# Kernel tuning notes

Measured on AMD Instinct MI355X. Metric: run time of the kernel, lower is better.

The kernel has to match this reference:

```python
import jax, jax.numpy as jnp
import numpy as np

M_NODES = 49152  # HEALPix nside=64


def setup_inputs() -> dict:
    key = jax.random.key(0)
    ks = jax.random.split(key, 7)
    N, M, Fin, Fout, K, dm = 16, M_NODES, 32, 64, 5, 1
    E = 8 * M
    x = jax.random.normal(ks[0], (N, M, Fin), dtype=jnp.float32)
    # sparse Laplacian in COO form; small values keep Chebyshev recursion stable
    edge_vals = jax.random.normal(ks[1], (E,), dtype=jnp.float32) * 0.2
    edge_rows = jax.random.randint(ks[2], (E,), 0, M, dtype=jnp.int32)
    edge_cols = jax.random.randint(ks[3], (E,), 0, M, dtype=jnp.int32)
    dkernel = jax.random.normal(ks[4], (Fin, dm, K), dtype=jnp.float32) * (2.0 / K) ** 0.5
    pkernel = jax.random.normal(ks[5], (Fout, Fin * dm), dtype=jnp.float32) * (2.0 / (Fin * dm)) ** 0.5
    bias = jax.random.normal(ks[6], (1, 1, Fout), dtype=jnp.float32) * 0.01
    return {"x": x, "edge_vals": edge_vals, "dkernel": dkernel,
            "pkernel": pkernel, "bias": bias,
            "edge_rows": edge_rows, "edge_cols": edge_cols}


def reference(x, edge_vals, dkernel, pkernel, bias, edge_rows, edge_cols):
    N, M, Fin = x.shape
    _, dm, K = dkernel.shape
    Fout = pkernel.shape[0]

    def spmm(v):  # L @ v with L in COO, v: [M, C]
        return jax.ops.segment_sum(edge_vals[:, None] * v[edge_cols], edge_rows,
                                   num_segments=M)

    # x0: [M, N*Fin]
    x0 = jnp.transpose(x, (1, 0, 2)).reshape(M, N * Fin)
    stack = [x0]
    if K > 1:
        x1 = spmm(x0)
        stack.append(x1)
    for k in range(2, K):  # Chebyshev recursion T_k = 2 L T_{k-1} - T_{k-2}
        x2 = 2.0 * spmm(x1) - x0
        stack.append(x2)
        x0, x1 = x1, x2
    xs = jnp.stack(stack, axis=0)                      # [K, M, N*Fin]
    xs = xs.reshape(K, M, N, Fin)
    xs = jnp.transpose(xs, (3, 0, 2, 1)).reshape(Fin, K, N * M)
    y = jnp.einsum('fdk,fkp->fdp', dkernel, xs)        # depthwise: [Fin, dm, N*M]
    y = y.reshape(Fin * dm, N * M)
    y = pkernel @ y                                    # pointwise: [Fout, N*M]
    y = y.T.reshape(N, M, Fout)
    y = y + bias
    return jax.nn.relu(y)
```

## Files before the change

### kernel.cpp

```cpp
#include <hip/hip_runtime.h>


#define M_NODES 49152
#define FIN 32
#define KCH 5
#define FOUT 64
#define NB 16

typedef unsigned int u32;
typedef unsigned short u16;
typedef short bf16x8 __attribute__((ext_vector_type(8)));
typedef float f32x4 __attribute__((ext_vector_type(4)));

__device__ __forceinline__ float bflo(u32 w) { union { float f; u32 i; } v; v.i = w << 16; return v.f; }
__device__ __forceinline__ float bfhi(u32 w) { union { float f; u32 i; } v; v.i = w & 0xffff0000u; return v.f; }
__device__ __forceinline__ u32 f2bf(float f) {
    union { float f; u32 i; } v; v.f = f;
    u32 r = v.i + 0x7fffu + ((v.i >> 16) & 1u);
    return r >> 16;
}
__device__ __forceinline__ u32 pack2(float a, float b) { return f2bf(a) | (f2bf(b) << 16); }

__device__ __forceinline__ void stage_row(const uint4* gsrc, uint4* ldst) {
    __builtin_amdgcn_global_load_lds(
        (const __attribute__((address_space(1))) unsigned int*)gsrc,
        (__attribute__((address_space(3))) unsigned int*)ldst, 16, 0, 0);
}

__global__ void scatter_kernel(const int* __restrict__ rows, const int* __restrict__ cols,
                               const float* __restrict__ vals, int* __restrict__ cnt,
                               int2* __restrict__ ell, int E4) {
    int e = blockIdx.x * 256 + threadIdx.x;
    if (e < E4) {
        int4 r = ((const int4*)rows)[e];
        int4 c = ((const int4*)cols)[e];
        float4 v = ((const float4*)vals)[e];
        int pos;
        pos = atomicAdd(&cnt[r.x], 1); if (pos < 32) ell[(size_t)r.x * 32 + pos] = (int2){c.x, __float_as_int(v.x)};
        pos = atomicAdd(&cnt[r.y], 1); if (pos < 32) ell[(size_t)r.y * 32 + pos] = (int2){c.y, __float_as_int(v.y)};
        pos = atomicAdd(&cnt[r.z], 1); if (pos < 32) ell[(size_t)r.z * 32 + pos] = (int2){c.z, __float_as_int(v.z)};
        pos = atomicAdd(&cnt[r.w], 1); if (pos < 32) ell[(size_t)r.w * 32 + pos] = (int2){c.w, __float_as_int(v.w)};
    }
}

__global__ __launch_bounds__(256) void cast_transpose_kernel(
    const float* __restrict__ x, uint4* __restrict__ T0, int M) {
    int m = blockIdx.x * 4 + (threadIdx.x >> 6);
    int l = threadIdx.x & 63;
    int n = l >> 2;
    int f0 = (l & 3) * 8;
    const f32x4* xp = (const f32x4*)(x + ((size_t)n * M + m) * FIN + f0);
    f32x4 a = __builtin_nontemporal_load(xp);
    f32x4 b = __builtin_nontemporal_load(xp + 1);
    uint4 o;
    o.x = pack2(a[0], a[1]); o.y = pack2(a[2], a[3]);
    o.z = pack2(b[0], b[1]); o.w = pack2(b[2], b[3]);
    T0[(size_t)m * 64 + l] = o;
}

__global__ void wprep_kernel(const float* __restrict__ dk, const float* __restrict__ pk,
                             u16* __restrict__ W) {
    int t = blockIdx.x * 256 + threadIdx.x;
    if (t < FOUT * KCH * FIN) {
        int fo = t / (KCH * FIN);
        int kf = t % (KCH * FIN);
        int kc = kf / FIN;
        int f  = kf % FIN;
        W[fo * (KCH * FIN) + kf] = (u16)f2bf(pk[fo * FIN + f] * dk[f * KCH + kc]);
    }
}

__device__ __forceinline__ void acc8(float* r, uint4 g, float v) {
    r[0] = fmaf(v, bflo(g.x), r[0]); r[1] = fmaf(v, bfhi(g.x), r[1]);
    r[2] = fmaf(v, bflo(g.y), r[2]); r[3] = fmaf(v, bfhi(g.y), r[3]);
    r[4] = fmaf(v, bflo(g.z), r[4]); r[5] = fmaf(v, bfhi(g.z), r[5]);
    r[6] = fmaf(v, bflo(g.w), r[6]); r[7] = fmaf(v, bfhi(g.w), r[7]);
}

template<int FIRST>
__global__ __launch_bounds__(256) void spmm_kernel(
    const uint4* __restrict__ Tin, const uint4* __restrict__ Tprev, uint4* __restrict__ Tout,
    const int* __restrict__ deg, const int2* __restrict__ ell, int M) {
    int w = __builtin_amdgcn_readfirstlane((int)(threadIdx.x >> 6));
    int l = threadIdx.x & 63;
    int rA = blockIdx.x * 8 + w * 2;
    int rB = rA + 1;
    int dA = deg[rA]; if (dA > 32) dA = 32;
    int dB = deg[rB]; if (dB > 32) dB = 32;
    const int2* eA = ell + (size_t)rA * 32;
    const int2* eB = ell + (size_t)rB * 32;
    uint4 pA, pB;
    if (!FIRST) {
        pA = Tprev[(size_t)rA * 64 + l];
        pB = Tprev[(size_t)rB * 64 + l];
    }
    float a[8] = {0.f, 0.f, 0.f, 0.f, 0.f, 0.f, 0.f, 0.f};
    float b[8] = {0.f, 0.f, 0.f, 0.f, 0.f, 0.f, 0.f, 0.f};
    int dmax = dA > dB ? dA : dB;
    for (int s = 0; s < dmax; s += 8) {
        int cA = dA - s, cB = dB - s;
        int2 edA[8], edB[8];
        uint4 gA[8], gB[8];
        #pragma unroll
        for (int j = 0; j < 8; ++j) if (j < cA) edA[j] = eA[s + j];
        #pragma unroll
        for (int j = 0; j < 8; ++j) if (j < cB) edB[j] = eB[s + j];
        #pragma unroll
        for (int j = 0; j < 8; ++j) if (j < cA) gA[j] = Tin[(size_t)edA[j].x * 64 + l];
        #pragma unroll
        for (int j = 0; j < 8; ++j) if (j < cB) gB[j] = Tin[(size_t)edB[j].x * 64 + l];
        #pragma unroll
        for (int j = 0; j < 8; ++j) if (j < cA) acc8(a, gA[j], __int_as_float(edA[j].y));
        #pragma unroll
        for (int j = 0; j < 8; ++j) if (j < cB) acc8(b, gB[j], __int_as_float(edB[j].y));
    }
    if (!FIRST) {
        a[0] = fmaf(2.f, a[0], -bflo(pA.x)); a[1] = fmaf(2.f, a[1], -bfhi(pA.x));
        a[2] = fmaf(2.f, a[2], -bflo(pA.y)); a[3] = fmaf(2.f, a[3], -bfhi(pA.y));
        a[4] = fmaf(2.f, a[4], -bflo(pA.z)); a[5] = fmaf(2.f, a[5], -bfhi(pA.z));
        a[6] = fmaf(2.f, a[6], -bflo(pA.w)); a[7] = fmaf(2.f, a[7], -bfhi(pA.w));
        b[0] = fmaf(2.f, b[0], -bflo(pB.x)); b[1] = fmaf(2.f, b[1], -bfhi(pB.x));
        b[2] = fmaf(2.f, b[2], -bflo(pB.y)); b[3] = fmaf(2.f, b[3], -bfhi(pB.y));
        b[4] = fmaf(2.f, b[4], -bflo(pB.z)); b[5] = fmaf(2.f, b[5], -bfhi(pB.z));
        b[6] = fmaf(2.f, b[6], -bflo(pB.w)); b[7] = fmaf(2.f, b[7], -bfhi(pB.w));
    }
    uint4 oA, oB;
    oA.x = pack2(a[0], a[1]); oA.y = pack2(a[2], a[3]);
    oA.z = pack2(a[4], a[5]); oA.w = pack2(a[6], a[7]);
    oB.x = pack2(b[0], b[1]); oB.y = pack2(b[2], b[3]);
    oB.z = pack2(b[4], b[5]); oB.w = pack2(b[6], b[7]);
    Tout[(size_t)rA * 64 + l] = oA;
    Tout[(size_t)rB * 64 + l] = oB;
}

__global__ __launch_bounds__(256) void pw_mfma_kernel(
    const uint4* __restrict__ T, const uint4* __restrict__ W4,
    const float* __restrict__ bias, float* __restrict__ out, int M) {
    __shared__ uint4 lds4[5 * 1024];
    int t = threadIdx.x;
    int w = t >> 6;
    int l = t & 63;
    int lr = l & 15;
    int lg = l >> 4;
    int m0 = blockIdx.x * 16;
    const size_t kstride = (size_t)M * 64;

    bf16x8 bfr[KCH][4];
    #pragma unroll
    for (int kc = 0; kc < KCH; ++kc)
        #pragma unroll
        for (int fo = 0; fo < 4; ++fo) {
            uint4 wv = W4[(fo * 16 + lr) * 20 + kc * 4 + lg];
            bfr[kc][fo] = *(bf16x8*)&wv;
        }
    f32x4 acc[4][4];
    #pragma unroll
    for (int fo = 0; fo < 4; ++fo) {
        float bv = bias[fo * 16 + lr];
        #pragma unroll
        for (int nn = 0; nn < 4; ++nn)
            acc[nn][fo] = (f32x4){bv, bv, bv, bv};
    }

    #pragma unroll
    for (int kc = 0; kc < KCH; ++kc) {
        #pragma unroll
        for (int i = 0; i < 4; ++i) {
            int row = w * 4 + i;
            const uint4* gsrc = T + (size_t)kc * kstride + (size_t)(m0 + row) * 64
                                  + (l ^ (row & 7));
            stage_row(gsrc, &lds4[kc * 1024 + row * 64]);
        }
    }
    __syncthreads();

    #pragma unroll
    for (int kc = 0; kc < KCH; ++kc) {
        #pragma unroll
        for (int nn = 0; nn < 4; ++nn) {
            int n = w * 4 + nn;
            uint4 a = lds4[kc * 1024 + lr * 64 + ((n * 4 + lg) ^ (lr & 7))];
            bf16x8 af = *(bf16x8*)&a;
            #pragma unroll
            for (int fo = 0; fo < 4; ++fo)
                acc[nn][fo] = __builtin_amdgcn_mfma_f32_16x16x32_bf16(af, bfr[kc][fo], acc[nn][fo], 0, 0, 0);
        }
    }
    __syncthreads();

    float* zone = (float*)lds4 + w * 1088;
    #pragma unroll
    for (int nn = 0; nn < 4; ++nn) {
        int n = w * 4 + nn;
        #pragma unroll
        for (int fo = 0; fo < 4; ++fo)
            #pragma unroll
            for (int rr = 0; rr < 4; ++rr)
                zone[(lg * 4 + rr) * 68 + fo * 16 + lr] = acc[nn][fo][rr];
        #pragma unroll
        for (int i = 0; i < 4; ++i) {
            int mrow = i * 4 + lg;
            f32x4 v = *(const f32x4*)&zone[mrow * 68 + lr * 4];
            v[0] = fmaxf(v[0], 0.f); v[1] = fmaxf(v[1], 0.f);
            v[2] = fmaxf(v[2], 0.f); v[3] = fmaxf(v[3], 0.f);
            f32x4* op = (f32x4*)(out + ((size_t)n * M + m0 + mrow) * FOUT + lr * 4);
            __builtin_nontemporal_store(v, op);
        }
    }
}

extern "C" void kernel_launch(void* const* d_in, const int* in_sizes, int n_in,
                              void* d_out, int out_size, void* d_ws, size_t ws_size,
                              hipStream_t stream) {
    const float* x         = (const float*)d_in[0];
    const float* edge_vals = (const float*)d_in[1];
    const float* dk        = (const float*)d_in[2];
    const float* pk        = (const float*)d_in[3];
    const float* bias      = (const float*)d_in[4];
    const int*   erow      = (const int*)d_in[5];
    const int*   ecol      = (const int*)d_in[6];
    float* out = (float*)d_out;

    const int M = M_NODES;
    const int E = in_sizes[1];

    size_t t_words = (size_t)M * 64;
    uint4* T    = (uint4*)d_ws;
    u16*   W    = (u16*)(T + 5 * t_words);
    int*   deg  = (int*)(W + FOUT * KCH * FIN);
    int2*  ell  = (int2*)(deg + M);

    uint4* T0 = T;
    uint4* T1 = T + 1 * t_words;
    uint4* T2 = T + 2 * t_words;
    uint4* T3 = T + 3 * t_words;
    uint4* T4 = T + 4 * t_words;

    hipMemsetAsync(deg, 0, (size_t)M * sizeof(int), stream);
    scatter_kernel<<<(E / 4 + 255) / 256, 256, 0, stream>>>(erow, ecol, edge_vals, deg, ell, E / 4);

    cast_transpose_kernel<<<M / 4, 256, 0, stream>>>(x, T0, M);
    wprep_kernel<<<(FOUT * KCH * FIN + 255) / 256, 256, 0, stream>>>(dk, pk, W);

    spmm_kernel<1><<<M / 8, 256, 0, stream>>>(T0, T0, T1, deg, ell, M);
    spmm_kernel<0><<<M / 8, 256, 0, stream>>>(T1, T0, T2, deg, ell, M);
    spmm_kernel<0><<<M / 8, 256, 0, stream>>>(T2, T1, T3, deg, ell, M);
    spmm_kernel<0><<<M / 8, 256, 0, stream>>>(T3, T2, T4, deg, ell, M);

    pw_mfma_kernel<<<M / 16, 256, 0, stream>>>(T, (const uint4*)W, bias, out, M);
}
```

Before: 415.8 us.

## Reorder T into batch-group slices and split SpMM by group for cache locality

Changes the Chebyshev T buffers from node-major [M][N*Fin] to batch-slice-major [N][M][Fin] layout, so the input cast becomes a plain elementwise cast with no transpose. Each SpMM pass is split into two launches over halves of the batch, so the gathered working set per launch is smaller and more likely to stay in cache. SpMM now spreads a row's edges over four lane groups and reduces them with shuffles. ELL entries are packed into 32 bits as a 16-bit column plus a bf16 value, which truncates edge values to bf16 and limits column indices to 16 bits. The pointwise kernel's staging addresses are adjusted to read the new layout.

```diff
diff --git a/kernel.cpp b/kernel.cpp
--- a/kernel.cpp
+++ b/kernel.cpp
@@ -11,6 +11,7 @@
 typedef unsigned short u16;
 typedef short bf16x8 __attribute__((ext_vector_type(8)));
 typedef float f32x4 __attribute__((ext_vector_type(4)));
+typedef unsigned int u32x4 __attribute__((ext_vector_type(4)));
 
 __device__ __forceinline__ float bflo(u32 w) { union { float f; u32 i; } v; v.i = w << 16; return v.f; }
 __device__ __forceinline__ float bfhi(u32 w) { union { float f; u32 i; } v; v.i = w & 0xffff0000u; return v.f; }
@@ -20,6 +21,11 @@
     return r >> 16;
 }
 __device__ __forceinline__ u32 pack2(float a, float b) { return f2bf(a) | (f2bf(b) << 16); }
+__device__ __forceinline__ u32 cvtpk(float lo, float hi) {
+    u32 r;
+    asm("v_cvt_pk_bf16_f32 %0, %1, %2" : "=v"(r) : "v"(lo), "v"(hi));
+    return r;
+}
 
 __device__ __forceinline__ void stage_row(const uint4* gsrc, uint4* ldst) {
     __builtin_amdgcn_global_load_lds(
@@ -29,33 +35,32 @@
 
 __global__ void scatter_kernel(const int* __restrict__ rows, const int* __restrict__ cols,
                                const float* __restrict__ vals, int* __restrict__ cnt,
-                               int2* __restrict__ ell, int E4) {
+                               u32* __restrict__ ell, int E4) {
     int e = blockIdx.x * 256 + threadIdx.x;
     if (e < E4) {
         int4 r = ((const int4*)rows)[e];
         int4 c = ((const int4*)cols)[e];
         float4 v = ((const float4*)vals)[e];
         int pos;
-        pos = atomicAdd(&cnt[r.x], 1); if (pos < 32) ell[(size_t)r.x * 32 + pos] = (int2){c.x, __float_as_int(v.x)};
-        pos = atomicAdd(&cnt[r.y], 1); if (pos < 32) ell[(size_t)r.y * 32 + pos] = (int2){c.y, __float_as_int(v.y)};
-        pos = atomicAdd(&cnt[r.z], 1); if (pos < 32) ell[(size_t)r.z * 32 + pos] = (int2){c.z, __float_as_int(v.z)};
-        pos = atomicAdd(&cnt[r.w], 1); if (pos < 32) ell[(size_t)r.w * 32 + pos] = (int2){c.w, __float_as_int(v.w)};
-    }
-}
-
-__global__ __launch_bounds__(256) void cast_transpose_kernel(
-    const float* __restrict__ x, uint4* __restrict__ T0, int M) {
-    int m = blockIdx.x * 4 + (threadIdx.x >> 6);
-    int l = threadIdx.x & 63;
-    int n = l >> 2;
-    int f0 = (l & 3) * 8;
-    const f32x4* xp = (const f32x4*)(x + ((size_t)n * M + m) * FIN + f0);
-    f32x4 a = __builtin_nontemporal_load(xp);
-    f32x4 b = __builtin_nontemporal_load(xp + 1);
-    uint4 o;
-    o.x = pack2(a[0], a[1]); o.y = pack2(a[2], a[3]);
-    o.z = pack2(b[0], b[1]); o.w = pack2(b[2], b[3]);
-    T0[(size_t)m * 64 + l] = o;
+        pos = atomicAdd(&cnt[r.x], 1); if (pos < 32) ell[(size_t)r.x * 32 + pos] = (u32)(c.x & 0xFFFF) | (f2bf(v.x) << 16);
+        pos = atomicAdd(&cnt[r.y], 1); if (pos < 32) ell[(size_t)r.y * 32 + pos] = (u32)(c.y & 0xFFFF) | (f2bf(v.y) << 16);
+        pos = atomicAdd(&cnt[r.z], 1); if (pos < 32) ell[(size_t)r.z * 32 + pos] = (u32)(c.z & 0xFFFF) | (f2bf(v.z) << 16);
+        pos = atomicAdd(&cnt[r.w], 1); if (pos < 32) ell[(size_t)r.w * 32 + pos] = (u32)(c.w & 0xFFFF) | (f2bf(v.w) << 16);
+    }
+}
+
+__global__ __launch_bounds__(256) void cast_kernel(const float* __restrict__ x,
+                                                   uint4* __restrict__ T0, int n8) {
+    int i = blockIdx.x * 256 + threadIdx.x;
+    if (i < n8) {
+        const f32x4* xp = (const f32x4*)(x + (size_t)i * 8);
+        f32x4 a = __builtin_nontemporal_load(xp);
+        f32x4 b = __builtin_nontemporal_load(xp + 1);
+        uint4 o;
+        o.x = pack2(a[0], a[1]); o.y = pack2(a[2], a[3]);
+        o.z = pack2(b[0], b[1]); o.w = pack2(b[2], b[3]);
+        T0[i] = o;
+    }
 }
 
 __global__ void wprep_kernel(const float* __restrict__ dk, const float* __restrict__ pk,
@@ -70,67 +75,61 @@
     }
 }
 
-__device__ __forceinline__ void acc8(float* r, uint4 g, float v) {
-    r[0] = fmaf(v, bflo(g.x), r[0]); r[1] = fmaf(v, bfhi(g.x), r[1]);
-    r[2] = fmaf(v, bflo(g.y), r[2]); r[3] = fmaf(v, bfhi(g.y), r[3]);
-    r[4] = fmaf(v, bflo(g.z), r[4]); r[5] = fmaf(v, bfhi(g.z), r[5]);
-    r[6] = fmaf(v, bflo(g.w), r[6]); r[7] = fmaf(v, bfhi(g.w), r[7]);
-}
-
 template<int FIRST>
 __global__ __launch_bounds__(256) void spmm_kernel(
     const uint4* __restrict__ Tin, const uint4* __restrict__ Tprev, uint4* __restrict__ Tout,
-    const int* __restrict__ deg, const int2* __restrict__ ell, int M) {
-    int w = __builtin_amdgcn_readfirstlane((int)(threadIdx.x >> 6));
-    int l = threadIdx.x & 63;
-    int rA = blockIdx.x * 8 + w * 2;
-    int rB = rA + 1;
-    int dA = deg[rA]; if (dA > 32) dA = 32;
-    int dB = deg[rB]; if (dB > 32) dB = 32;
-    const int2* eA = ell + (size_t)rA * 32;
-    const int2* eB = ell + (size_t)rB * 32;
-    uint4 pA, pB;
-    if (!FIRST) {
-        pA = Tprev[(size_t)rA * 64 + l];
-        pB = Tprev[(size_t)rB * 64 + l];
-    }
-    float a[8] = {0.f, 0.f, 0.f, 0.f, 0.f, 0.f, 0.f, 0.f};
-    float b[8] = {0.f, 0.f, 0.f, 0.f, 0.f, 0.f, 0.f, 0.f};
-    int dmax = dA > dB ? dA : dB;
-    for (int s = 0; s < dmax; s += 8) {
-        int cA = dA - s, cB = dB - s;
-        int2 edA[8], edB[8];
-        uint4 gA[8], gB[8];
-        #pragma unroll
-        for (int j = 0; j < 8; ++j) if (j < cA) edA[j] = eA[s + j];
-        #pragma unroll
-        for (int j = 0; j < 8; ++j) if (j < cB) edB[j] = eB[s + j];
-        #pragma unroll
-        for (int j = 0; j < 8; ++j) if (j < cA) gA[j] = Tin[(size_t)edA[j].x * 64 + l];
-        #pragma unroll
-        for (int j = 0; j < 8; ++j) if (j < cB) gB[j] = Tin[(size_t)edB[j].x * 64 + l];
-        #pragma unroll
-        for (int j = 0; j < 8; ++j) if (j < cA) acc8(a, gA[j], __int_as_float(edA[j].y));
-        #pragma unroll
-        for (int j = 0; j < 8; ++j) if (j < cB) acc8(b, gB[j], __int_as_float(edB[j].y));
-    }
-    if (!FIRST) {
-        a[0] = fmaf(2.f, a[0], -bflo(pA.x)); a[1] = fmaf(2.f, a[1], -bfhi(pA.x));
-        a[2] = fmaf(2.f, a[2], -bflo(pA.y)); a[3] = fmaf(2.f, a[3], -bfhi(pA.y));
-        a[4] = fmaf(2.f, a[4], -bflo(pA.z)); a[5] = fmaf(2.f, a[5], -bfhi(pA.z));
-        a[6] = fmaf(2.f, a[6], -bflo(pA.w)); a[7] = fmaf(2.f, a[7], -bfhi(pA.w));
-        b[0] = fmaf(2.f, b[0], -bflo(pB.x)); b[1] = fmaf(2.f, b[1], -bfhi(pB.x));
-        b[2] = fmaf(2.f, b[2], -bflo(pB.y)); b[3] = fmaf(2.f, b[3], -bfhi(pB.y));
-        b[4] = fmaf(2.f, b[4], -bflo(pB.z)); b[5] = fmaf(2.f, b[5], -bfhi(pB.z));
-        b[6] = fmaf(2.f, b[6], -bflo(pB.w)); b[7] = fmaf(2.f, b[7], -bfhi(pB.w));
-    }
-    uint4 oA, oB;
-    oA.x = pack2(a[0], a[1]); oA.y = pack2(a[2], a[3]);
-    oA.z = pack2(a[4], a[5]); oA.w = pack2(a[6], a[7]);
-    oB.x = pack2(b[0], b[1]); oB.y = pack2(b[2], b[3]);
-    oB.z = pack2(b[4], b[5]); oB.w = pack2(b[6], b[7]);
-    Tout[(size_t)rA * 64 + l] = oA;
-    Tout[(size_t)rB * 64 + l] = oB;
+    const int* __restrict__ deg, const u32* __restrict__ ell, int gbase) {
+    const int M = M_NODES;
+    int t = threadIdx.x;
+    int l = t & 63;
+    int w = t >> 6;
+    int g = gbase + (blockIdx.x & 7);
+    int r = ((blockIdx.x >> 3) << 4) + (w << 2) + (l >> 4);
+    int j = (l >> 2) & 3;
+    int c = l & 3;
+    int d = deg[r]; if (d > 32) d = 32;
+    const u32* erow = ell + ((size_t)r << 5);
+    size_t sbase = (size_t)g * M * 4;
+    size_t srow  = sbase + (size_t)r * 4;
+
+    u32x4 p;
+    if (!FIRST) p = __builtin_nontemporal_load((const u32x4*)&Tprev[srow + c]);
+
+    float acc[8] = {0.f, 0.f, 0.f, 0.f, 0.f, 0.f, 0.f, 0.f};
+    for (int s = 0; s < d; s += 4) {
+        int mine = s + j;
+        u32 desc = 0;
+        if (mine < d) desc = __builtin_nontemporal_load(&erow[mine]);
+        float v = bfhi(desc);
+        int col = desc & 0xFFFF;
+        uint4 gv = {0, 0, 0, 0};
+        if (mine < d) gv = Tin[sbase + (size_t)col * 4 + c];
+        acc[0] = fmaf(v, bflo(gv.x), acc[0]); acc[1] = fmaf(v, bfhi(gv.x), acc[1]);
+        acc[2] = fmaf(v, bflo(gv.y), acc[2]); acc[3] = fmaf(v, bfhi(gv.y), acc[3]);
+        acc[4] = fmaf(v, bflo(gv.z), acc[4]); acc[5] = fmaf(v, bfhi(gv.z), acc[5]);
+        acc[6] = fmaf(v, bflo(gv.w), acc[6]); acc[7] = fmaf(v, bfhi(gv.w), acc[7]);
+    }
+    #pragma unroll
+    for (int q = 0; q < 8; ++q) acc[q] += __shfl_xor(acc[q], 4, 64);
+    #pragma unroll
+    for (int q = 0; q < 8; ++q) acc[q] += __shfl_xor(acc[q], 8, 64);
+
+    if (j == 0) {
+        float rr[8];
+        if (FIRST) {
+            #pragma unroll
+            for (int q = 0; q < 8; ++q) rr[q] = acc[q];
+        } else {
+            rr[0] = fmaf(2.f, acc[0], -bflo(p[0])); rr[1] = fmaf(2.f, acc[1], -bfhi(p[0]));
+            rr[2] = fmaf(2.f, acc[2], -bflo(p[1])); rr[3] = fmaf(2.f, acc[3], -bfhi(p[1]));
+            rr[4] = fmaf(2.f, acc[4], -bflo(p[2])); rr[5] = fmaf(2.f, acc[5], -bfhi(p[2]));
+            rr[6] = fmaf(2.f, acc[6], -bflo(p[3])); rr[7] = fmaf(2.f, acc[7], -bfhi(p[3]));
+        }
+        u32x4 o;
+        o[0] = cvtpk(rr[0], rr[1]); o[1] = cvtpk(rr[2], rr[3]);
+        o[2] = cvtpk(rr[4], rr[5]); o[3] = cvtpk(rr[6], rr[7]);
+        __builtin_nontemporal_store(o, (u32x4*)&Tout[srow + c]);
+    }
 }
 
 __global__ __launch_bounds__(256) void pw_mfma_kernel(
@@ -143,7 +142,8 @@
     int lr = l & 15;
     int lg = l >> 4;
     int m0 = blockIdx.x * 16;
-    const size_t kstride = (size_t)M * 64;
+    const size_t tslice = (size_t)M * 4;
+    const size_t kstride = tslice * 16;
 
     bf16x8 bfr[KCH][4];
     #pragma unroll
@@ -164,11 +164,12 @@
 
     #pragma unroll
     for (int kc = 0; kc < KCH; ++kc) {
+        const uint4* tk = T + (size_t)kc * kstride;
         #pragma unroll
         for (int i = 0; i < 4; ++i) {
             int row = w * 4 + i;
-            const uint4* gsrc = T + (size_t)kc * kstride + (size_t)(m0 + row) * 64
-                                  + (l ^ (row & 7));
+            int q = l ^ (row & 7);
+            const uint4* gsrc = tk + (size_t)(q >> 2) * tslice + (size_t)(m0 + row) * 4 + (q & 3);
             stage_row(gsrc, &lds4[kc * 1024 + row * 64]);
         }
     }
@@ -224,28 +225,34 @@
     const int M = M_NODES;
     const int E = in_sizes[1];
 
-    size_t t_words = (size_t)M * 64;
+    size_t t_u4 = (size_t)M * 4 * 16;
     uint4* T    = (uint4*)d_ws;
-    u16*   W    = (u16*)(T + 5 * t_words);
+    u16*   W    = (u16*)(T + 5 * t_u4);
     int*   deg  = (int*)(W + FOUT * KCH * FIN);
-    int2*  ell  = (int2*)(deg + M);
+    u32*   ell  = (u32*)(deg + M);
 
     uint4* T0 = T;
-    uint4* T1 = T + 1 * t_words;
-    uint4* T2 = T + 2 * t_words;
-    uint4* T3 = T + 3 * t_words;
-    uint4* T4 = T + 4 * t_words;
+    uint4* T1 = T + 1 * t_u4;
+    uint4* T2 = T + 2 * t_u4;
+    uint4* T3 = T + 3 * t_u4;
+    uint4* T4 = T + 4 * t_u4;
 
     hipMemsetAsync(deg, 0, (size_t)M * sizeof(int), stream);
     scatter_kernel<<<(E / 4 + 255) / 256, 256, 0, stream>>>(erow, ecol, edge_vals, deg, ell, E / 4);
 
-    cast_transpose_kernel<<<M / 4, 256, 0, stream>>>(x, T0, M);
+    int n8 = NB * M * FIN / 8;
+    cast_kernel<<<(n8 + 255) / 256, 256, 0, stream>>>(x, T0, n8);
     wprep_kernel<<<(FOUT * KCH * FIN + 255) / 256, 256, 0, stream>>>(dk, pk, W);
 
-    spmm_kernel<1><<<M / 8, 256, 0, stream>>>(T0, T0, T1, deg, ell, M);
-    spmm_kernel<0><<<M / 8, 256, 0, stream>>>(T1, T0, T2, deg, ell, M);
-    spmm_kernel<0><<<M / 8, 256, 0, stream>>>(T2, T1, T3, deg, ell, M);
-    spmm_kernel<0><<<M / 8, 256, 0, stream>>>(T3, T2, T4, deg, ell, M);
+    const int sgrid = 8 * (M / 16);
+    spmm_kernel<1><<<sgrid, 256, 0, stream>>>(T0, T0, T1, deg, ell, 0);
+    spmm_kernel<1><<<sgrid, 256, 0, stream>>>(T0, T0, T1, deg, ell, 8);
+    spmm_kernel<0><<<sgrid, 256, 0, stream>>>(T1, T0, T2, deg, ell, 0);
+    spmm_kernel<0><<<sgrid, 256, 0, stream>>>(T1, T0, T2, deg, ell, 8);
+    spmm_kernel<0><<<sgrid, 256, 0, stream>>>(T2, T1, T3, deg, ell, 0);
+    spmm_kernel<0><<<sgrid, 256, 0, stream>>>(T2, T1, T3, deg, ell, 8);
+    spmm_kernel<0><<<sgrid, 256, 0, stream>>>(T3, T2, T4, deg, ell, 0);
+    spmm_kernel<0><<<sgrid, 256, 0, stream>>>(T3, T2, T4, deg, ell, 8);
 
     pw_mfma_kernel<<<M / 16, 256, 0, stream>>>(T, (const uint4*)W, bias, out, M);
 }
```

New measurement: 690.5 us. 1.66x slower.

## Pack ELL entries into 32 bits and restructure pointwise MFMA per output slice

Applied to the files above, without the earlier changes.

ELL entries shrink from an int2 (column, fp32 value) to one u32 holding a 16-bit column index and a bf16 value, halving index traffic in the four SpMM passes. This relies on M fitting in 16 bits, which holds since 49152 < 65536, and it rounds the Laplacian values to bf16. The pointwise MFMA kernel drops the LDS staging of all K slices. Each wave now owns 16 output features and loops over the 16 batch entries, loading A fragments straight from global memory and using a small double-buffered LDS zone for the output transpose. This cuts LDS use and register pressure, at the cost of possibly less coalesced A loads.

```diff
diff --git a/kernel.cpp b/kernel.cpp
--- a/kernel.cpp
+++ b/kernel.cpp
@@ -21,25 +21,19 @@
 }
 __device__ __forceinline__ u32 pack2(float a, float b) { return f2bf(a) | (f2bf(b) << 16); }
 
-__device__ __forceinline__ void stage_row(const uint4* gsrc, uint4* ldst) {
-    __builtin_amdgcn_global_load_lds(
-        (const __attribute__((address_space(1))) unsigned int*)gsrc,
-        (__attribute__((address_space(3))) unsigned int*)ldst, 16, 0, 0);
-}
-
 __global__ void scatter_kernel(const int* __restrict__ rows, const int* __restrict__ cols,
                                const float* __restrict__ vals, int* __restrict__ cnt,
-                               int2* __restrict__ ell, int E4) {
+                               u32* __restrict__ ell, int E4) {
     int e = blockIdx.x * 256 + threadIdx.x;
     if (e < E4) {
         int4 r = ((const int4*)rows)[e];
         int4 c = ((const int4*)cols)[e];
         float4 v = ((const float4*)vals)[e];
         int pos;
-        pos = atomicAdd(&cnt[r.x], 1); if (pos < 32) ell[(size_t)r.x * 32 + pos] = (int2){c.x, __float_as_int(v.x)};
-        pos = atomicAdd(&cnt[r.y], 1); if (pos < 32) ell[(size_t)r.y * 32 + pos] = (int2){c.y, __float_as_int(v.y)};
-        pos = atomicAdd(&cnt[r.z], 1); if (pos < 32) ell[(size_t)r.z * 32 + pos] = (int2){c.z, __float_as_int(v.z)};
-        pos = atomicAdd(&cnt[r.w], 1); if (pos < 32) ell[(size_t)r.w * 32 + pos] = (int2){c.w, __float_as_int(v.w)};
+        pos = atomicAdd(&cnt[r.x], 1); if (pos < 32) ell[(size_t)r.x * 32 + pos] = (u32)(c.x & 0xFFFF) | (f2bf(v.x) << 16);
+        pos = atomicAdd(&cnt[r.y], 1); if (pos < 32) ell[(size_t)r.y * 32 + pos] = (u32)(c.y & 0xFFFF) | (f2bf(v.y) << 16);
+        pos = atomicAdd(&cnt[r.z], 1); if (pos < 32) ell[(size_t)r.z * 32 + pos] = (u32)(c.z & 0xFFFF) | (f2bf(v.z) << 16);
+        pos = atomicAdd(&cnt[r.w], 1); if (pos < 32) ell[(size_t)r.w * 32 + pos] = (u32)(c.w & 0xFFFF) | (f2bf(v.w) << 16);
     }
 }
 
@@ -80,15 +74,15 @@
 template<int FIRST>
 __global__ __launch_bounds__(256) void spmm_kernel(
     const uint4* __restrict__ Tin, const uint4* __restrict__ Tprev, uint4* __restrict__ Tout,
-    const int* __restrict__ deg, const int2* __restrict__ ell, int M) {
+    const int* __restrict__ deg, const u32* __restrict__ ell, int M) {
     int w = __builtin_amdgcn_readfirstlane((int)(threadIdx.x >> 6));
     int l = threadIdx.x & 63;
     int rA = blockIdx.x * 8 + w * 2;
     int rB = rA + 1;
     int dA = deg[rA]; if (dA > 32) dA = 32;
     int dB = deg[rB]; if (dB > 32) dB = 32;
-    const int2* eA = ell + (size_t)rA * 32;
-    const int2* eB = ell + (size_t)rB * 32;
+    const u32* eA = ell + ((size_t)rA << 5);
+    const u32* eB = ell + ((size_t)rB << 5);
     uint4 pA, pB;
     if (!FIRST) {
         pA = Tprev[(size_t)rA * 64 + l];
@@ -99,20 +93,20 @@
     int dmax = dA > dB ? dA : dB;
     for (int s = 0; s < dmax; s += 8) {
         int cA = dA - s, cB = dB - s;
-        int2 edA[8], edB[8];
+        u32 edA[8], edB[8];
         uint4 gA[8], gB[8];
         #pragma unroll
         for (int j = 0; j < 8; ++j) if (j < cA) edA[j] = eA[s + j];
         #pragma unroll
         for (int j = 0; j < 8; ++j) if (j < cB) edB[j] = eB[s + j];
         #pragma unroll
-        for (int j = 0; j < 8; ++j) if (j < cA) gA[j] = Tin[(size_t)edA[j].x * 64 + l];
-        #pragma unroll
-        for (int j = 0; j < 8; ++j) if (j < cB) gB[j] = Tin[(size_t)edB[j].x * 64 + l];
-        #pragma unroll
-        for (int j = 0; j < 8; ++j) if (j < cA) acc8(a, gA[j], __int_as_float(edA[j].y));
-        #pragma unroll
-        for (int j = 0; j < 8; ++j) if (j < cB) acc8(b, gB[j], __int_as_float(edB[j].y));
+        for (int j = 0; j < 8; ++j) if (j < cA) gA[j] = Tin[(size_t)(edA[j] & 0xFFFF) * 64 + l];
+        #pragma unroll
+        for (int j = 0; j < 8; ++j) if (j < cB) gB[j] = Tin[(size_t)(edB[j] & 0xFFFF) * 64 + l];
+        #pragma unroll
+        for (int j = 0; j < 8; ++j) if (j < cA) acc8(a, gA[j], bfhi(edA[j]));
+        #pragma unroll
+        for (int j = 0; j < 8; ++j) if (j < cB) acc8(b, gB[j], bfhi(edB[j]));
     }
     if (!FIRST) {
         a[0] = fmaf(2.f, a[0], -bflo(pA.x)); a[1] = fmaf(2.f, a[1], -bfhi(pA.x));
@@ -136,76 +130,47 @@
 __global__ __launch_bounds__(256) void pw_mfma_kernel(
     const uint4* __restrict__ T, const uint4* __restrict__ W4,
     const float* __restrict__ bias, float* __restrict__ out, int M) {
-    __shared__ uint4 lds4[5 * 1024];
+    __shared__ float zone[4 * 640];
     int t = threadIdx.x;
     int w = t >> 6;
     int l = t & 63;
     int lr = l & 15;
     int lg = l >> 4;
     int m0 = blockIdx.x * 16;
+    int fo0 = w * 16;
     const size_t kstride = (size_t)M * 64;
 
-    bf16x8 bfr[KCH][4];
-    #pragma unroll
-    for (int kc = 0; kc < KCH; ++kc)
-        #pragma unroll
-        for (int fo = 0; fo < 4; ++fo) {
-            uint4 wv = W4[(fo * 16 + lr) * 20 + kc * 4 + lg];
-            bfr[kc][fo] = *(bf16x8*)&wv;
-        }
-    f32x4 acc[4][4];
-    #pragma unroll
-    for (int fo = 0; fo < 4; ++fo) {
-        float bv = bias[fo * 16 + lr];
-        #pragma unroll
-        for (int nn = 0; nn < 4; ++nn)
-            acc[nn][fo] = (f32x4){bv, bv, bv, bv};
-    }
-
+    bf16x8 bfr[KCH];
     #pragma unroll
     for (int kc = 0; kc < KCH; ++kc) {
-        #pragma unroll
-        for (int i = 0; i < 4; ++i) {
-            int row = w * 4 + i;
-            const uint4* gsrc = T + (size_t)kc * kstride + (size_t)(m0 + row) * 64
-                                  + (l ^ (row & 7));
-            stage_row(gsrc, &lds4[kc * 1024 + row * 64]);
-        }
-    }
-    __syncthreads();
-
-    #pragma unroll
-    for (int kc = 0; kc < KCH; ++kc) {
-        #pragma unroll
-        for (int nn = 0; nn < 4; ++nn) {
-            int n = w * 4 + nn;
-            uint4 a = lds4[kc * 1024 + lr * 64 + ((n * 4 + lg) ^ (lr & 7))];
-            bf16x8 af = *(bf16x8*)&a;
-            #pragma unroll
-            for (int fo = 0; fo < 4; ++fo)
-                acc[nn][fo] = __builtin_amdgcn_mfma_f32_16x16x32_bf16(af, bfr[kc][fo], acc[nn][fo], 0, 0, 0);
-        }
-    }
-    __syncthreads();
-
-    float* zone = (float*)lds4 + w * 1088;
-    #pragma unroll
-    for (int nn = 0; nn < 4; ++nn) {
-        int n = w * 4 + nn;
-        #pragma unroll
-        for (int fo = 0; fo < 4; ++fo)
-            #pragma unroll
-            for (int rr = 0; rr < 4; ++rr)
-                zone[(lg * 4 + rr) * 68 + fo * 16 + lr] = acc[nn][fo][rr];
-        #pragma unroll
-        for (int i = 0; i < 4; ++i) {
-            int mrow = i * 4 + lg;
-            f32x4 v = *(const f32x4*)&zone[mrow * 68 + lr * 4];
-            v[0] = fmaxf(v[0], 0.f); v[1] = fmaxf(v[1], 0.f);
-            v[2] = fmaxf(v[2], 0.f); v[3] = fmaxf(v[3], 0.f);
-            f32x4* op = (f32x4*)(out + ((size_t)n * M + m0 + mrow) * FOUT + lr * 4);
-            __builtin_nontemporal_store(v, op);
-        }
+        uint4 wv = W4[(fo0 + lr) * 20 + kc * 4 + lg];
+        bfr[kc] = *(bf16x8*)&wv;
+    }
+    float bv = bias[fo0 + lr];
+    const uint4* abase = T + (size_t)(m0 + lr) * 64 + lg;
+    float* zbase = zone + w * 640;
+    int zr = l >> 2;
+    int zc = (l & 3) * 4;
+
+    #pragma unroll 2
+    for (int n = 0; n < NB; ++n) {
+        uint4 a[KCH];
+        #pragma unroll
+        for (int kc = 0; kc < KCH; ++kc)
+            a[kc] = abase[(size_t)kc * kstride + n * 4];
+        f32x4 acc = {bv, bv, bv, bv};
+        #pragma unroll
+        for (int kc = 0; kc < KCH; ++kc)
+            acc = __builtin_amdgcn_mfma_f32_16x16x32_bf16(*(bf16x8*)&a[kc], bfr[kc], acc, 0, 0, 0);
+        float* zw = zbase + (n & 1) * 320;
+        #pragma unroll
+        for (int rr = 0; rr < 4; ++rr)
+            zw[(lg * 4 + rr) * 20 + lr] = acc[rr];
+        f32x4 v = *(const f32x4*)&zw[zr * 20 + zc];
+        v[0] = fmaxf(v[0], 0.f); v[1] = fmaxf(v[1], 0.f);
+        v[2] = fmaxf(v[2], 0.f); v[3] = fmaxf(v[3], 0.f);
+        f32x4* op = (f32x4*)(out + ((size_t)n * M + m0 + zr) * FOUT + fo0 + zc);
+        __builtin_nontemporal_store(v, op);
     }
 }
 
@@ -228,7 +193,7 @@
     uint4* T    = (uint4*)d_ws;
     u16*   W    = (u16*)(T + 5 * t_words);
     int*   deg  = (int*)(W + FOUT * KCH * FIN);
-    int2*  ell  = (int2*)(deg + M);
+    u32*   ell  = (u32*)(deg + M);
 
     uint4* T0 = T;
     uint4* T1 = T + 1 * t_words;
```

New measurement: 461.2 us. 1.11x slower.

## Pack ELL entries into 32-bit index+bf16 value and widen pointwise blocks to 512

Applied to the files above, without the earlier changes.

Each ELL entry shrinks from an int2 to a single 32-bit word holding a 16-bit column index and a bf16 edge value. This halves the edge-list bytes the four SpMM passes read. The pointwise MFMA kernel now runs 512 threads per block, so each wave handles two batch rows instead of four, and weight fragments are loaded per Chebyshev order rather than held all at once, which lowers register pressure. The trade-offs are a coarser edge value in bf16 and column indices that only fit because M is at most 65536.

```diff
diff --git a/kernel.cpp b/kernel.cpp
--- a/kernel.cpp
+++ b/kernel.cpp
@@ -29,17 +29,17 @@
 
 __global__ void scatter_kernel(const int* __restrict__ rows, const int* __restrict__ cols,
                                const float* __restrict__ vals, int* __restrict__ cnt,
-                               int2* __restrict__ ell, int E4) {
+                               u32* __restrict__ ell, int E4) {
     int e = blockIdx.x * 256 + threadIdx.x;
     if (e < E4) {
         int4 r = ((const int4*)rows)[e];
         int4 c = ((const int4*)cols)[e];
         float4 v = ((const float4*)vals)[e];
         int pos;
-        pos = atomicAdd(&cnt[r.x], 1); if (pos < 32) ell[(size_t)r.x * 32 + pos] = (int2){c.x, __float_as_int(v.x)};
-        pos = atomicAdd(&cnt[r.y], 1); if (pos < 32) ell[(size_t)r.y * 32 + pos] = (int2){c.y, __float_as_int(v.y)};
-        pos = atomicAdd(&cnt[r.z], 1); if (pos < 32) ell[(size_t)r.z * 32 + pos] = (int2){c.z, __float_as_int(v.z)};
-        pos = atomicAdd(&cnt[r.w], 1); if (pos < 32) ell[(size_t)r.w * 32 + pos] = (int2){c.w, __float_as_int(v.w)};
+        pos = atomicAdd(&cnt[r.x], 1); if (pos < 32) ell[(size_t)r.x * 32 + pos] = (u32)(c.x & 0xFFFF) | (f2bf(v.x) << 16);
+        pos = atomicAdd(&cnt[r.y], 1); if (pos < 32) ell[(size_t)r.y * 32 + pos] = (u32)(c.y & 0xFFFF) | (f2bf(v.y) << 16);
+        pos = atomicAdd(&cnt[r.z], 1); if (pos < 32) ell[(size_t)r.z * 32 + pos] = (u32)(c.z & 0xFFFF) | (f2bf(v.z) << 16);
+        pos = atomicAdd(&cnt[r.w], 1); if (pos < 32) ell[(size_t)r.w * 32 + pos] = (u32)(c.w & 0xFFFF) | (f2bf(v.w) << 16);
     }
 }
 
@@ -80,15 +80,15 @@
 template<int FIRST>
 __global__ __launch_bounds__(256) void spmm_kernel(
     const uint4* __restrict__ Tin, const uint4* __restrict__ Tprev, uint4* __restrict__ Tout,
-    const int* __restrict__ deg, const int2* __restrict__ ell, int M) {
+    const int* __restrict__ deg, const u32* __restrict__ ell, int M) {
     int w = __builtin_amdgcn_readfirstlane((int)(threadIdx.x >> 6));
     int l = threadIdx.x & 63;
     int rA = blockIdx.x * 8 + w * 2;
     int rB = rA + 1;
     int dA = deg[rA]; if (dA > 32) dA = 32;
     int dB = deg[rB]; if (dB > 32) dB = 32;
-    const int2* eA = ell + (size_t)rA * 32;
-    const int2* eB = ell + (size_t)rB * 32;
+    const u32* eA = ell + ((size_t)rA << 5);
+    const u32* eB = ell + ((size_t)rB << 5);
     uint4 pA, pB;
     if (!FIRST) {
         pA = Tprev[(size_t)rA * 64 + l];
@@ -99,20 +99,20 @@
     int dmax = dA > dB ? dA : dB;
     for (int s = 0; s < dmax; s += 8) {
         int cA = dA - s, cB = dB - s;
-        int2 edA[8], edB[8];
+        u32 edA[8], edB[8];
         uint4 gA[8], gB[8];
         #pragma unroll
         for (int j = 0; j < 8; ++j) if (j < cA) edA[j] = eA[s + j];
         #pragma unroll
         for (int j = 0; j < 8; ++j) if (j < cB) edB[j] = eB[s + j];
         #pragma unroll
-        for (int j = 0; j < 8; ++j) if (j < cA) gA[j] = Tin[(size_t)edA[j].x * 64 + l];
-        #pragma unroll
-        for (int j = 0; j < 8; ++j) if (j < cB) gB[j] = Tin[(size_t)edB[j].x * 64 + l];
-        #pragma unroll
-        for (int j = 0; j < 8; ++j) if (j < cA) acc8(a, gA[j], __int_as_float(edA[j].y));
-        #pragma unroll
-        for (int j = 0; j < 8; ++j) if (j < cB) acc8(b, gB[j], __int_as_float(edB[j].y));
+        for (int j = 0; j < 8; ++j) if (j < cA) gA[j] = Tin[(size_t)(edA[j] & 0xFFFF) * 64 + l];
+        #pragma unroll
+        for (int j = 0; j < 8; ++j) if (j < cB) gB[j] = Tin[(size_t)(edB[j] & 0xFFFF) * 64 + l];
+        #pragma unroll
+        for (int j = 0; j < 8; ++j) if (j < cA) acc8(a, gA[j], bfhi(edA[j]));
+        #pragma unroll
+        for (int j = 0; j < 8; ++j) if (j < cB) acc8(b, gB[j], bfhi(edB[j]));
     }
     if (!FIRST) {
         a[0] = fmaf(2.f, a[0], -bflo(pA.x)); a[1] = fmaf(2.f, a[1], -bfhi(pA.x));
@@ -133,7 +133,7 @@
     Tout[(size_t)rB * 64 + l] = oB;
 }
 
-__global__ __launch_bounds__(256) void pw_mfma_kernel(
+__global__ __launch_bounds__(512, 4) void pw_mfma_kernel(
     const uint4* __restrict__ T, const uint4* __restrict__ W4,
     const float* __restrict__ bias, float* __restrict__ out, int M) {
     __shared__ uint4 lds4[5 * 1024];
@@ -145,53 +145,51 @@
     int m0 = blockIdx.x * 16;
     const size_t kstride = (size_t)M * 64;
 
-    bf16x8 bfr[KCH][4];
-    #pragma unroll
-    for (int kc = 0; kc < KCH; ++kc)
-        #pragma unroll
-        for (int fo = 0; fo < 4; ++fo) {
-            uint4 wv = W4[(fo * 16 + lr) * 20 + kc * 4 + lg];
-            bfr[kc][fo] = *(bf16x8*)&wv;
-        }
-    f32x4 acc[4][4];
-    #pragma unroll
-    for (int fo = 0; fo < 4; ++fo) {
-        float bv = bias[fo * 16 + lr];
-        #pragma unroll
-        for (int nn = 0; nn < 4; ++nn)
-            acc[nn][fo] = (f32x4){bv, bv, bv, bv};
-    }
-
     #pragma unroll
     for (int kc = 0; kc < KCH; ++kc) {
         #pragma unroll
-        for (int i = 0; i < 4; ++i) {
-            int row = w * 4 + i;
+        for (int i = 0; i < 2; ++i) {
+            int row = w * 2 + i;
             const uint4* gsrc = T + (size_t)kc * kstride + (size_t)(m0 + row) * 64
                                   + (l ^ (row & 7));
             stage_row(gsrc, &lds4[kc * 1024 + row * 64]);
         }
     }
+
+    f32x4 acc[2][4];
+    #pragma unroll
+    for (int fo = 0; fo < 4; ++fo) {
+        float bv = bias[fo * 16 + lr];
+        #pragma unroll
+        for (int nn = 0; nn < 2; ++nn)
+            acc[nn][fo] = (f32x4){bv, bv, bv, bv};
+    }
     __syncthreads();
 
     #pragma unroll
     for (int kc = 0; kc < KCH; ++kc) {
-        #pragma unroll
-        for (int nn = 0; nn < 4; ++nn) {
-            int n = w * 4 + nn;
+        bf16x8 bfr[4];
+        #pragma unroll
+        for (int fo = 0; fo < 4; ++fo) {
+            uint4 wv = W4[(fo * 16 + lr) * 20 + kc * 4 + lg];
+            bfr[fo] = *(bf16x8*)&wv;
+        }
+        #pragma unroll
+        for (int nn = 0; nn < 2; ++nn) {
+            int n = w * 2 + nn;
             uint4 a = lds4[kc * 1024 + lr * 64 + ((n * 4 + lg) ^ (lr & 7))];
             bf16x8 af = *(bf16x8*)&a;
             #pragma unroll
             for (int fo = 0; fo < 4; ++fo)
-                acc[nn][fo] = __builtin_amdgcn_mfma_f32_16x16x32_bf16(af, bfr[kc][fo], acc[nn][fo], 0, 0, 0);
+                acc[nn][fo] = __builtin_amdgcn_mfma_f32_16x16x32_bf16(af, bfr[fo], acc[nn][fo], 0, 0, 0);
         }
     }
     __syncthreads();
 
     float* zone = (float*)lds4 + w * 1088;
     #pragma unroll
-    for (int nn = 0; nn < 4; ++nn) {
-        int n = w * 4 + nn;
+    for (int nn = 0; nn < 2; ++nn) {
+        int n = w * 2 + nn;
         #pragma unroll
         for (int fo = 0; fo < 4; ++fo)
             #pragma unroll
@@ -228,7 +226,7 @@
     uint4* T    = (uint4*)d_ws;
     u16*   W    = (u16*)(T + 5 * t_words);
     int*   deg  = (int*)(W + FOUT * KCH * FIN);
-    int2*  ell  = (int2*)(deg + M);
+    u32*   ell  = (u32*)(deg + M);
 
     uint4* T0 = T;
     uint4* T1 = T + 1 * t_words;
@@ -247,5 +245,5 @@
     spmm_kernel<0><<<M / 8, 256, 0, stream>>>(T2, T1, T3, deg, ell, M);
     spmm_kernel<0><<<M / 8, 256, 0, stream>>>(T3, T2, T4, deg, ell, M);
 
-    pw_mfma_kernel<<<M / 16, 256, 0, stream>>>(T, (const uint4*)W, bias, out, M);
-}
+    pw_mfma_kernel<<<M / 16, 512, 0, stream>>>(T, (const uint4*)W, bias, out, M);
+}
```

Measured after the change: 416.9 us. No clear change (+0.3%).
